# Optimization experiments

Measured on AMD Instinct MI355X. Metric: run time of the kernel, lower is better.

## Reference

```python
import jax, jax.numpy as jnp
import numpy as np

# Module / input configuration
N, H, W, C = 4, 64, 64, 128
G = 4                    # groups
GC = C // G              # group_channels = 32 (power of 2)
KS = 3                   # kernel_size (also dw_kernel_size)
P = KS * KS              # sampling points per group
STRIDE, PAD, DIL = 1, 1, 1
OFFSET_SCALE = 1.0
LN_EPS = 1e-6
DW_PAD = (KS - 1) // 2


def dcnv3_core(x, offset, mask):
    """DCNv3 sampling core (matches _C.dcnv3_forward / InternImage pytorch core).
    x: (N,H,W,C) projected input; offset: (N,Ho,Wo,G*P*2); mask: (N,Ho,Wo,G*P)."""
    n, h, w, _ = x.shape
    xp = jnp.pad(x, ((0, 0), (PAD, PAD), (PAD, PAD), (0, 0)))
    H_in, W_in = h + 2 * PAD, w + 2 * PAD
    Ho = (H_in - (DIL * (KS - 1) + 1)) // STRIDE + 1
    Wo = (W_in - (DIL * (KS - 1) + 1)) // STRIDE + 1
    # reference points in normalized padded coords (align_corners=False convention)
    base = (DIL * (KS - 1)) // 2 + 0.5
    ref_x = (base + jnp.arange(Wo, dtype=x.dtype) * STRIDE) / W_in
    ref_y = (base + jnp.arange(Ho, dtype=x.dtype) * STRIDE) / H_in
    rx, ry = jnp.broadcast_arrays(ref_x[None, :], ref_y[:, None])
    ref = jnp.stack([rx, ry], -1)                      # (Ho,Wo,2), (x,y)
    # dilation grid, w-index-major ordering as in reference impl
    gx = (jnp.arange(KS, dtype=x.dtype) * DIL - (DIL * (KS - 1)) // 2) / W_in
    gy = (jnp.arange(KS, dtype=x.dtype) * DIL - (DIL * (KS - 1)) // 2) / H_in
    gxm, gym = jnp.meshgrid(gx, gy, indexing='ij')
    grid = jnp.stack([gxm, gym], -1).reshape(P, 2)     # (P,2)
    norm = jnp.array([W_in, H_in], x.dtype)
    loc = (ref[None, :, :, None, None, :]
           + grid[None, None, None, None, :, :] * OFFSET_SCALE
           + offset.reshape(n, Ho, Wo, G, P, 2) * OFFSET_SCALE / norm)
    # normalized -> pixel coords (grid_sample align_corners=False): p = loc*size - 0.5
    px = loc[..., 0] * W_in - 0.5                      # (N,Ho,Wo,G,P)
    py = loc[..., 1] * H_in - 0.5
    xg = xp.reshape(n, H_in, W_in, G, GC)
    x0 = jnp.floor(px)
    y0 = jnp.floor(py)
    bi = jnp.arange(n).reshape(n, 1, 1, 1, 1)
    gi = jnp.arange(G).reshape(1, 1, 1, G, 1)

    def gather(iy, ix):
        valid = (ix >= 0) & (ix < W_in) & (iy >= 0) & (iy < H_in)
        ixc = jnp.clip(ix, 0, W_in - 1).astype(jnp.int32)
        iyc = jnp.clip(iy, 0, H_in - 1).astype(jnp.int32)
        v = xg[bi, iyc, ixc, gi]                       # (N,Ho,Wo,G,P,GC)
        return jnp.where(valid[..., None], v, jnp.zeros((), x.dtype))

    wx1 = px - x0
    wy1 = py - y0
    wx0 = 1.0 - wx1
    wy0 = 1.0 - wy1
    val = (gather(y0, x0) * (wy0 * wx0)[..., None]
           + gather(y0, x0 + 1) * (wy0 * wx1)[..., None]
           + gather(y0 + 1, x0) * (wy1 * wx0)[..., None]
           + gather(y0 + 1, x0 + 1) * (wy1 * wx1)[..., None])
    out = (val * mask.reshape(n, Ho, Wo, G, P, 1)).sum(4)   # (N,Ho,Wo,G,GC)
    return out.reshape(n, Ho, Wo, G * GC)


def setup_inputs() -> dict:
    key = jax.random.key(0)
    ks = jax.random.split(key, 8)
    s = lambda fan: 1.0 / np.sqrt(fan)
    return {
        'input': jax.random.normal(ks[0], (N, H, W, C), jnp.float32),
        'w_in': jax.random.normal(ks[1], (C, C), jnp.float32) * s(C),
        'b_in': jnp.zeros((C,), jnp.float32),
        'w_out': jax.random.normal(ks[2], (C, C), jnp.float32) * s(C),
        'b_out': jnp.zeros((C,), jnp.float32),
        'w_off': jax.random.normal(ks[3], (C, G * P * 2), jnp.float32) * 0.01,
        'b_off': jnp.zeros((G * P * 2,), jnp.float32),
        'w_mask': jax.random.normal(ks[4], (C, G * P), jnp.float32) * 0.01,
        'b_mask': jnp.zeros((G * P,), jnp.float32),
        'dw_kernel': jax.random.normal(ks[5], (KS, KS, 1, C), jnp.float32) * s(KS * KS),
        'dw_bias': jnp.zeros((C,), jnp.float32),
        'ln_gamma': jnp.ones((C,), jnp.float32),
        'ln_beta': jnp.zeros((C,), jnp.float32),
    }


def reference(input, w_in, b_in, w_out, b_out, w_off, b_off, w_mask, b_mask,
              dw_kernel, dw_bias, ln_gamma, ln_beta):
    # input_proj
    x = input @ w_in + b_in
    # dw_conv branch: depthwise conv -> LayerNorm (channels_last, eps=1e-6) -> GELU (exact)
    x1 = jax.lax.conv_general_dilated(
        input, dw_kernel, (1, 1), [(DW_PAD, DW_PAD), (DW_PAD, DW_PAD)],
        feature_group_count=C,
        dimension_numbers=('NHWC', 'HWIO', 'NHWC')) + dw_bias
    mu = x1.mean(-1, keepdims=True)
    var = ((x1 - mu) ** 2).mean(-1, keepdims=True)
    x1 = (x1 - mu) * jax.lax.rsqrt(var + LN_EPS) * ln_gamma + ln_beta
    x1 = jax.nn.gelu(x1, approximate=False)
    # offsets and softmax-normalized modulation mask
    offset = x1 @ w_off + b_off
    mask = jax.nn.softmax((x1 @ w_mask + b_mask).reshape(N, H, W, G, P), axis=-1)
    mask = mask.reshape(N, H, W, G * P)
    # deformable sampling core
    x = dcnv3_core(x, offset, mask)
    # output_proj
    return x @ w_out + b_out
```

## Files before the change

### kernel.cpp

```cpp
#include <hip/hip_runtime.h>
#include <math.h>

#define NB 4
#define HH 64
#define WW 64
#define CC 128
#define GG 4
#define GC 32
#define PP 9
#define MPIX (NB*HH*WW)
#define PIXC ((size_t)MPIX*CC)

__global__ __launch_bounds__(256) void pack_offmask_w(
    const float* __restrict__ w_off, const float* __restrict__ b_off,
    const float* __restrict__ w_mask, const float* __restrict__ b_mask,
    float* __restrict__ Bpack, float* __restrict__ bpack)
{
    int e = blockIdx.x * 256 + threadIdx.x;
    if (e < 128 * 128) {
        int k = e >> 7, j = e & 127;
        float v = 0.f;
        if (j < 72)       v = w_off[k * 72 + j];
        else if (j < 108) v = w_mask[k * 36 + (j - 72)];
        Bpack[e] = v;
    } else if (e < 128 * 128 + 128) {
        int j = e - 128 * 128;
        float v = 0.f;
        if (j < 72)       v = b_off[j];
        else if (j < 108) v = b_mask[j - 72];
        bpack[j] = v;
    }
}

__global__ __launch_bounds__(256) void gemm_m128(
    const float* __restrict__ A, const float* __restrict__ B,
    const float* __restrict__ bias, float* __restrict__ C)
{
    __shared__ float sA[32][68];
    __shared__ float sB[32][128];

    const int t  = threadIdx.x;
    const int tr = t >> 4;
    const int tc = t & 15;
    const int row0 = blockIdx.x << 6;

    float acc[4][8];
#pragma unroll
    for (int r = 0; r < 4; r++)
#pragma unroll
        for (int c = 0; c < 8; c++) acc[r][c] = 0.f;

    for (int kc = 0; kc < 128; kc += 32) {
#pragma unroll
        for (int i = 0; i < 2; i++) {
            int idx = t + i * 256;
            int r  = idx >> 3;
            int c4 = (idx & 7) << 2;
            float4 v = *(const float4*)(A + (size_t)(row0 + r) * 128 + kc + c4);
            sA[c4 + 0][r] = v.x; sA[c4 + 1][r] = v.y;
            sA[c4 + 2][r] = v.z; sA[c4 + 3][r] = v.w;
        }
#pragma unroll
        for (int i = 0; i < 4; i++) {
            int idx = t + i * 256;
            int r  = idx >> 5;
            int c4 = (idx & 31) << 2;
            *(float4*)(&sB[r][c4]) = *(const float4*)(B + (size_t)(kc + r) * 128 + c4);
        }
        __syncthreads();
#pragma unroll
        for (int k = 0; k < 32; k++) {
            float4 a  = *(const float4*)(&sA[k][tr << 2]);
            float4 b0 = *(const float4*)(&sB[k][tc << 2]);
            float4 b1 = *(const float4*)(&sB[k][64 + (tc << 2)]);
            float ar[4] = {a.x, a.y, a.z, a.w};
            float br[8] = {b0.x, b0.y, b0.z, b0.w, b1.x, b1.y, b1.z, b1.w};
#pragma unroll
            for (int r = 0; r < 4; r++)
#pragma unroll
                for (int c = 0; c < 8; c++)
                    acc[r][c] = fmaf(ar[r], br[c], acc[r][c]);
        }
        __syncthreads();
    }

    const float4 bias0 = *(const float4*)(bias + (tc << 2));
    const float4 bias1 = *(const float4*)(bias + 64 + (tc << 2));
#pragma unroll
    for (int r = 0; r < 4; r++) {
        float* crow = C + (size_t)(row0 + (tr << 2) + r) * 128;
        float4 o0 = make_float4(acc[r][0] + bias0.x, acc[r][1] + bias0.y,
                                acc[r][2] + bias0.z, acc[r][3] + bias0.w);
        float4 o1 = make_float4(acc[r][4] + bias1.x, acc[r][5] + bias1.y,
                                acc[r][6] + bias1.z, acc[r][7] + bias1.w);
        *(float4*)(crow + (tc << 2)) = o0;
        *(float4*)(crow + 64 + (tc << 2)) = o1;
    }
}

__global__ __launch_bounds__(256) void dw_ln_gelu(
    const float* __restrict__ x, const float* __restrict__ kern,
    const float* __restrict__ kbias, const float* __restrict__ gamma,
    const float* __restrict__ beta, float* __restrict__ y)
{
    const int t  = threadIdx.x;
    const int pl = t >> 5;
    const int cq = (t & 31) << 2;
    const int pix = blockIdx.x * 8 + pl;
    const int w = pix & 63;
    const int h = (pix >> 6) & 63;
    const int b = pix >> 12;

    float4 acc = make_float4(0.f, 0.f, 0.f, 0.f);
#pragma unroll
    for (int kh = 0; kh < 3; kh++) {
        int hy = h + kh - 1;
        if (hy < 0 || hy > 63) continue;
#pragma unroll
        for (int kw = 0; kw < 3; kw++) {
            int wx = w + kw - 1;
            if (wx < 0 || wx > 63) continue;
            const float4 v  = *(const float4*)(x + (((size_t)((b * 64 + hy) * 64 + wx)) << 7) + cq);
            const float4 kv = *(const float4*)(kern + ((kh * 3 + kw) << 7) + cq);
            acc.x = fmaf(v.x, kv.x, acc.x);
            acc.y = fmaf(v.y, kv.y, acc.y);
            acc.z = fmaf(v.z, kv.z, acc.z);
            acc.w = fmaf(v.w, kv.w, acc.w);
        }
    }
    const float4 kb = *(const float4*)(kbias + cq);
    acc.x += kb.x; acc.y += kb.y; acc.z += kb.z; acc.w += kb.w;

    float s  = acc.x + acc.y + acc.z + acc.w;
    float s2 = acc.x * acc.x + acc.y * acc.y + acc.z * acc.z + acc.w * acc.w;
#pragma unroll
    for (int m = 16; m >= 1; m >>= 1) {
        s  += __shfl_xor(s, m);
        s2 += __shfl_xor(s2, m);
    }
    const float mu   = s * (1.f / 128.f);
    const float var  = s2 * (1.f / 128.f) - mu * mu;
    const float rstd = 1.f / sqrtf(var + 1e-6f);

    const float4 g  = *(const float4*)(gamma + cq);
    const float4 bb = *(const float4*)(beta + cq);
    float vv[4] = {acc.x, acc.y, acc.z, acc.w};
    float gg[4] = {g.x, g.y, g.z, g.w};
    float be[4] = {bb.x, bb.y, bb.z, bb.w};
    float4 outv;
    float* po = &outv.x;
#pragma unroll
    for (int i = 0; i < 4; i++) {
        float xh = (vv[i] - mu) * rstd * gg[i] + be[i];
        po[i] = 0.5f * xh * (1.f + erff(xh * 0.70710678118654752f));
    }
    *(float4*)(y + ((size_t)pix << 7) + cq) = outv;
}

__global__ __launch_bounds__(256) void dcn_sample(
    const float* __restrict__ xp, const float* __restrict__ om,
    float* __restrict__ out)
{
    const int t = threadIdx.x;
    const int q = t & 3;
    const int g = (t >> 2) & 3;
    const int pix = blockIdx.x * 16 + (t >> 4);
    const int w = pix & 63;
    const int h = (pix >> 6) & 63;
    const int b = pix >> 12;

    const float* ompix = om + ((size_t)pix << 7);

    float lg[9];
    float mx = -1e30f;
#pragma unroll
    for (int p = 0; p < 9; p++) {
        lg[p] = ompix[72 + g * 9 + p];
        mx = fmaxf(mx, lg[p]);
    }
    float sum = 0.f;
#pragma unroll
    for (int p = 0; p < 9; p++) { lg[p] = expf(lg[p] - mx); sum += lg[p]; }
    const float inv = 1.f / sum;

    float4 acc0 = make_float4(0.f, 0.f, 0.f, 0.f);
    float4 acc1 = make_float4(0.f, 0.f, 0.f, 0.f);
    const int chbase = g * 32 + q * 8;

#pragma unroll
    for (int p = 0; p < 9; p++) {
        const float ox = ompix[g * 18 + 2 * p];
        const float oy = ompix[g * 18 + 2 * p + 1];
        const float px = (float)(w + p / 3 - 1) + ox;
        const float py = (float)(h + p % 3 - 1) + oy;
        const float fx0 = floorf(px), fy0 = floorf(py);
        const int x0 = (int)fx0, y0 = (int)fy0;
        const float wx1 = px - fx0, wy1 = py - fy0;
        const float wx0 = 1.f - wx1, wy0 = 1.f - wy1;
        const float m = lg[p] * inv;
        const float cw[4] = {wy0 * wx0 * m, wy0 * wx1 * m, wy1 * wx0 * m, wy1 * wx1 * m};
        const int cx[4] = {x0, x0 + 1, x0, x0 + 1};
        const int cy[4] = {y0, y0, y0 + 1, y0 + 1};
#pragma unroll
        for (int c = 0; c < 4; c++) {
            const int xx = cx[c], yy = cy[c];
            if (xx >= 0 && xx < 64 && yy >= 0 && yy < 64) {
                const float* src = xp + (((size_t)((b * 64 + yy) * 64 + xx)) << 7) + chbase;
                const float4 v0 = *(const float4*)(src);
                const float4 v1 = *(const float4*)(src + 4);
                const float wt = cw[c];
                acc0.x = fmaf(v0.x, wt, acc0.x); acc0.y = fmaf(v0.y, wt, acc0.y);
                acc0.z = fmaf(v0.z, wt, acc0.z); acc0.w = fmaf(v0.w, wt, acc0.w);
                acc1.x = fmaf(v1.x, wt, acc1.x); acc1.y = fmaf(v1.y, wt, acc1.y);
                acc1.z = fmaf(v1.z, wt, acc1.z); acc1.w = fmaf(v1.w, wt, acc1.w);
            }
        }
    }
    float* dst = out + ((size_t)pix << 7) + chbase;
    *(float4*)(dst)     = acc0;
    *(float4*)(dst + 4) = acc1;
}

extern "C" void kernel_launch(void* const* d_in, const int* in_sizes, int n_in,
                              void* d_out, int out_size, void* d_ws, size_t ws_size,
                              hipStream_t stream)
{
    const float* input   = (const float*)d_in[0];
    const float* w_in    = (const float*)d_in[1];
    const float* b_in    = (const float*)d_in[2];
    const float* w_out   = (const float*)d_in[3];
    const float* b_out   = (const float*)d_in[4];
    const float* w_off   = (const float*)d_in[5];
    const float* b_off   = (const float*)d_in[6];
    const float* w_mask  = (const float*)d_in[7];
    const float* b_mask  = (const float*)d_in[8];
    const float* dw_kern = (const float*)d_in[9];
    const float* dw_bias = (const float*)d_in[10];
    const float* ln_g    = (const float*)d_in[11];
    const float* ln_b    = (const float*)d_in[12];
    float* out = (float*)d_out;

    float* ws      = (float*)d_ws;
    float* x_proj  = ws;
    float* x1      = ws + PIXC;
    float* offmask = ws + 2 * PIXC;
    float* Bpack   = ws + 3 * PIXC;
    float* bpack   = Bpack + 128 * 128;
    float* sampled = x1;

    pack_offmask_w<<<65, 256, 0, stream>>>(w_off, b_off, w_mask, b_mask, Bpack, bpack);
    gemm_m128<<<MPIX / 64, 256, 0, stream>>>(input, w_in, b_in, x_proj);
    dw_ln_gelu<<<MPIX / 8, 256, 0, stream>>>(input, dw_kern, dw_bias, ln_g, ln_b, x1);
    gemm_m128<<<MPIX / 64, 256, 0, stream>>>(x1, Bpack, bpack, offmask);
    dcn_sample<<<MPIX / 16, 256, 0, stream>>>(x_proj, offmask, sampled);
    gemm_m128<<<MPIX / 64, 256, 0, stream>>>(sampled, w_out, b_out, out);
}
```

Baseline: 154.1 us.

## Replace FP32 SIMT GEMMs with split-bf16 MFMA GEMMs

```diff
diff --git a/kernel.cpp b/kernel.cpp
--- a/kernel.cpp
+++ b/kernel.cpp
@@ -11,90 +11,125 @@
 #define MPIX (NB*HH*WW)
 #define PIXC ((size_t)MPIX*CC)
 
-__global__ __launch_bounds__(256) void pack_offmask_w(
+typedef short bf16x8 __attribute__((ext_vector_type(8)));
+typedef float f32x4  __attribute__((ext_vector_type(4)));
+
+__device__ __forceinline__ ushort f2bf(float f) {
+    uint u = __float_as_uint(f);
+    u += 0x7FFFu + ((u >> 16) & 1u);
+    return (ushort)(u >> 16);
+}
+__device__ __forceinline__ float bf2f(ushort h) {
+    return __uint_as_float(((uint)h) << 16);
+}
+
+__global__ __launch_bounds__(256) void prep_weights(
+    const float* __restrict__ w_in, const float* __restrict__ w_out,
     const float* __restrict__ w_off, const float* __restrict__ b_off,
     const float* __restrict__ w_mask, const float* __restrict__ b_mask,
-    float* __restrict__ Bpack, float* __restrict__ bpack)
-{
-    int e = blockIdx.x * 256 + threadIdx.x;
-    if (e < 128 * 128) {
-        int k = e >> 7, j = e & 127;
-        float v = 0.f;
-        if (j < 72)       v = w_off[k * 72 + j];
-        else if (j < 108) v = w_mask[k * 36 + (j - 72)];
-        Bpack[e] = v;
-    } else if (e < 128 * 128 + 128) {
-        int j = e - 128 * 128;
-        float v = 0.f;
-        if (j < 72)       v = b_off[j];
-        else if (j < 108) v = b_mask[j - 72];
-        bpack[j] = v;
-    }
-}
-
-__global__ __launch_bounds__(256) void gemm_m128(
-    const float* __restrict__ A, const float* __restrict__ B,
-    const float* __restrict__ bias, float* __restrict__ C)
-{
-    __shared__ float sA[32][68];
-    __shared__ float sB[32][128];
-
-    const int t  = threadIdx.x;
-    const int tr = t >> 4;
-    const int tc = t & 15;
-    const int row0 = blockIdx.x << 6;
-
-    float acc[4][8];
-#pragma unroll
-    for (int r = 0; r < 4; r++)
-#pragma unroll
-        for (int c = 0; c < 8; c++) acc[r][c] = 0.f;
-
-    for (int kc = 0; kc < 128; kc += 32) {
-#pragma unroll
-        for (int i = 0; i < 2; i++) {
-            int idx = t + i * 256;
-            int r  = idx >> 3;
-            int c4 = (idx & 7) << 2;
-            float4 v = *(const float4*)(A + (size_t)(row0 + r) * 128 + kc + c4);
-            sA[c4 + 0][r] = v.x; sA[c4 + 1][r] = v.y;
-            sA[c4 + 2][r] = v.z; sA[c4 + 3][r] = v.w;
-        }
-#pragma unroll
-        for (int i = 0; i < 4; i++) {
-            int idx = t + i * 256;
-            int r  = idx >> 5;
-            int c4 = (idx & 31) << 2;
-            *(float4*)(&sB[r][c4]) = *(const float4*)(B + (size_t)(kc + r) * 128 + c4);
-        }
-        __syncthreads();
-#pragma unroll
-        for (int k = 0; k < 32; k++) {
-            float4 a  = *(const float4*)(&sA[k][tr << 2]);
-            float4 b0 = *(const float4*)(&sB[k][tc << 2]);
-            float4 b1 = *(const float4*)(&sB[k][64 + (tc << 2)]);
-            float ar[4] = {a.x, a.y, a.z, a.w};
-            float br[8] = {b0.x, b0.y, b0.z, b0.w, b1.x, b1.y, b1.z, b1.w};
-#pragma unroll
-            for (int r = 0; r < 4; r++)
-#pragma unroll
-                for (int c = 0; c < 8; c++)
-                    acc[r][c] = fmaf(ar[r], br[c], acc[r][c]);
-        }
-        __syncthreads();
-    }
-
-    const float4 bias0 = *(const float4*)(bias + (tc << 2));
-    const float4 bias1 = *(const float4*)(bias + 64 + (tc << 2));
-#pragma unroll
-    for (int r = 0; r < 4; r++) {
-        float* crow = C + (size_t)(row0 + (tr << 2) + r) * 128;
-        float4 o0 = make_float4(acc[r][0] + bias0.x, acc[r][1] + bias0.y,
-                                acc[r][2] + bias0.z, acc[r][3] + bias0.w);
-        float4 o1 = make_float4(acc[r][4] + bias1.x, acc[r][5] + bias1.y,
-                                acc[r][6] + bias1.z, acc[r][7] + bias1.w);
-        *(float4*)(crow + (tc << 2)) = o0;
-        *(float4*)(crow + 64 + (tc << 2)) = o1;
+    ushort* __restrict__ BT, float* __restrict__ bpack)
+{
+    int idx = blockIdx.x * 256 + threadIdx.x;
+    if (idx < 3 * 128 * 32) {
+        int m  = idx >> 12;
+        int r  = idx & 4095;
+        int n  = r >> 5;
+        int k4 = (r & 31) << 2;
+        ushort h[4], l[4];
+#pragma unroll
+        for (int j = 0; j < 4; j++) {
+            int k = k4 + j;
+            float a;
+            if (m == 0)      a = w_in[k * 128 + n];
+            else if (m == 2) a = w_out[k * 128 + n];
+            else             a = (n < 72) ? w_off[k * 72 + n]
+                               : (n < 108 ? w_mask[k * 36 + (n - 72)] : 0.f);
+            ushort hh = f2bf(a);
+            h[j] = hh;
+            l[j] = f2bf(a - bf2f(hh));
+        }
+        ushort* dh = BT + m * 32768 + n * 128 + k4;
+        ushort* dl = dh + 16384;
+        *(ushort4*)dh = make_ushort4(h[0], h[1], h[2], h[3]);
+        *(ushort4*)dl = make_ushort4(l[0], l[1], l[2], l[3]);
+    } else if (idx < 3 * 128 * 32 + 128) {
+        int n = idx - 3 * 128 * 32;
+        bpack[n] = (n < 72) ? b_off[n] : (n < 108 ? b_mask[n - 72] : 0.f);
+    }
+}
+
+__global__ __launch_bounds__(256) void gemm_mfma(
+    const float* __restrict__ A, const ushort* __restrict__ BTh,
+    const ushort* __restrict__ BTl, const float* __restrict__ bias,
+    float* __restrict__ C)
+{
+    __shared__ ushort sB[2][128][128];
+
+    const int t = threadIdx.x;
+
+#pragma unroll
+    for (int i = 0; i < 16; i++) {
+        int c    = i * 256 + t;
+        int part = c >> 11;
+        int rem  = c & 2047;
+        int n    = rem >> 4;
+        int kc   = (rem & 15) << 3;
+        const ushort* src = (part ? BTl : BTh) + n * 128 + kc;
+        int4 v = *(const int4*)src;
+        int byte = part * 32768 + n * 256 + ((kc * 2) ^ ((n & 7) << 4));
+        *(int4*)((char*)sB + byte) = v;
+    }
+    __syncthreads();
+
+    const int w  = t >> 6;
+    const int l  = t & 63;
+    const int lr = l & 15;
+    const int lk = l >> 4;
+    const int row0 = (blockIdx.x << 6) + (w << 4);
+    const float* Arow = A + (size_t)(row0 + lr) * 128;
+
+    f32x4 acc[8];
+#pragma unroll
+    for (int nt = 0; nt < 8; nt++) acc[nt] = (f32x4){0.f, 0.f, 0.f, 0.f};
+
+#pragma unroll
+    for (int ks = 0; ks < 4; ks++) {
+        const float4 a0 = *(const float4*)(Arow + ks * 32 + lk * 8);
+        const float4 a1 = *(const float4*)(Arow + ks * 32 + lk * 8 + 4);
+        float av[8] = {a0.x, a0.y, a0.z, a0.w, a1.x, a1.y, a1.z, a1.w};
+        bf16x8 ah, al;
+#pragma unroll
+        for (int j = 0; j < 8; j++) {
+            ushort hh = f2bf(av[j]);
+            ah[j] = (short)hh;
+            al[j] = (short)f2bf(av[j] - bf2f(hh));
+        }
+        bf16x8 bh[8], bl[8];
+#pragma unroll
+        for (int nt = 0; nt < 8; nt++) {
+            int n = nt * 16 + lr;
+            int byte = n * 256 + (((ks * 32 + lk * 8) * 2) ^ ((n & 7) << 4));
+            bh[nt] = *(const bf16x8*)((const char*)sB + byte);
+            bl[nt] = *(const bf16x8*)((const char*)sB + 32768 + byte);
+        }
+#pragma unroll
+        for (int nt = 0; nt < 8; nt++)
+            acc[nt] = __builtin_amdgcn_mfma_f32_16x16x32_bf16(ah, bh[nt], acc[nt], 0, 0, 0);
+#pragma unroll
+        for (int nt = 0; nt < 8; nt++)
+            acc[nt] = __builtin_amdgcn_mfma_f32_16x16x32_bf16(al, bh[nt], acc[nt], 0, 0, 0);
+#pragma unroll
+        for (int nt = 0; nt < 8; nt++)
+            acc[nt] = __builtin_amdgcn_mfma_f32_16x16x32_bf16(ah, bl[nt], acc[nt], 0, 0, 0);
+    }
+
+#pragma unroll
+    for (int nt = 0; nt < 8; nt++) {
+        int col = nt * 16 + lr;
+        float bv = bias[col];
+#pragma unroll
+        for (int i = 0; i < 4; i++)
+            C[(size_t)(row0 + lk * 4 + i) * 128 + col] = acc[nt][i] + bv;
     }
 }
 
@@ -244,14 +279,15 @@
     float* x_proj  = ws;
     float* x1      = ws + PIXC;
     float* offmask = ws + 2 * PIXC;
-    float* Bpack   = ws + 3 * PIXC;
-    float* bpack   = Bpack + 128 * 128;
+    ushort* BT     = (ushort*)(ws + 3 * PIXC);
+    float* bpack   = (float*)(BT + 3 * 32768);
     float* sampled = x1;
 
-    pack_offmask_w<<<65, 256, 0, stream>>>(w_off, b_off, w_mask, b_mask, Bpack, bpack);
-    gemm_m128<<<MPIX / 64, 256, 0, stream>>>(input, w_in, b_in, x_proj);
+    prep_weights<<<49, 256, 0, stream>>>(w_in, w_out, w_off, b_off, w_mask, b_mask,
+                                         BT, bpack);
+    gemm_mfma<<<MPIX / 64, 256, 0, stream>>>(input, BT, BT + 16384, b_in, x_proj);
     dw_ln_gelu<<<MPIX / 8, 256, 0, stream>>>(input, dw_kern, dw_bias, ln_g, ln_b, x1);
-    gemm_m128<<<MPIX / 64, 256, 0, stream>>>(x1, Bpack, bpack, offmask);
+    gemm_mfma<<<MPIX / 64, 256, 0, stream>>>(x1, BT + 32768, BT + 49152, bpack, offmask);
     dcn_sample<<<MPIX / 16, 256, 0, stream>>>(x_proj, offmask, sampled);
-    gemm_m128<<<MPIX / 64, 256, 0, stream>>>(sampled, w_out, b_out, out);
-}
+    gemm_mfma<<<MPIX / 64, 256, 0, stream>>>(sampled, BT + 65536, BT + 81920, b_out, out);
+}
```

Result: faster. 134.5 us (-12.7%).
